# Kernel tuning notes

Measured on AMD Instinct MI355X. Metric: run time of the kernel, lower is better.

Reference implementation:

```python
import jax, jax.numpy as jnp
import numpy as np

D_MODEL = 1024
D_HIDDEN = 4096
NUM_EXPERT = 8
TOP_K = 2
B, N = 1, 8192


def setup_inputs() -> dict:
    key = jax.random.key(0)
    ks = jax.random.split(key, 8)
    s1 = 1.0 / np.sqrt(D_MODEL)
    s2 = 1.0 / np.sqrt(D_HIDDEN)
    return {
        "x": jax.random.normal(ks[0], (B, N, D_MODEL), jnp.float32),
        "expert_tokens": jax.random.normal(ks[1], (NUM_EXPERT, D_MODEL), jnp.float32),
        "W1": jax.random.normal(ks[2], (NUM_EXPERT, D_MODEL, D_HIDDEN), jnp.float32) * s1,
        "b1": jnp.zeros((NUM_EXPERT, D_HIDDEN), jnp.float32),
        "W2": jax.random.normal(ks[3], (NUM_EXPERT, D_HIDDEN, D_HIDDEN), jnp.float32) * s2,
        "b2": jnp.zeros((NUM_EXPERT, D_HIDDEN), jnp.float32),
        "W3": jax.random.normal(ks[4], (NUM_EXPERT, D_HIDDEN, D_MODEL), jnp.float32) * s2,
        "b3": jnp.zeros((NUM_EXPERT, D_MODEL), jnp.float32),
    }


def _expert_mlp(x, W1, b1, W2, b2, W3, b3):
    # Linear -> GELU (exact, matching torch nn.GELU) -> Linear -> GELU -> Linear
    h = jax.nn.gelu(jnp.einsum("bnd,dh->bnh", x, W1) + b1, approximate=False)
    h = jax.nn.gelu(jnp.einsum("bnh,hk->bnk", h, W2) + b2, approximate=False)
    return jnp.einsum("bnh,hd->bnd", h, W3) + b3


def reference(x, expert_tokens, W1, b1, W2, b2, W3, b3):
    # router scores: [B, N, E]
    scores = jnp.einsum("bnd,ed->bne", x, expert_tokens)
    _, topk_idx = jax.lax.top_k(scores, TOP_K)  # [B, N, TOP_K]
    outputs = jnp.zeros_like(x)
    num_expert = W1.shape[0]
    for i in range(num_expert):
        # gate weight = (# of top-k slots assigned to expert i) / top_k
        w = jnp.mean((topk_idx == i).astype(x.dtype), axis=-1, keepdims=True)
        y = _expert_mlp(x, W1[i], b1[i], W2[i], b2[i], W3[i], b3[i])
        outputs = outputs + y * w
    return outputs
```

## Files before the change

### kernel.cpp

```cpp
#include <hip/hip_runtime.h>
#include <stdint.h>

#define D_MODEL 1024
#define D_HID   4096
#define NEXP    8
#define NTOK    8192
#define TOTROW  (NTOK*2)

typedef unsigned short ushort_t;
typedef __attribute__((ext_vector_type(8))) short short8;
typedef __attribute__((ext_vector_type(4))) float f32x4;

static __device__ __forceinline__ ushort_t f2bf(float f) {
    union { float f; uint32_t u; } v; v.f = f;
    uint32_t u = v.u;
    uint32_t r = (u + 0x7FFFu + ((u >> 16) & 1u)) >> 16;
    return (ushort_t)r;
}
static __device__ __forceinline__ float bf2f(ushort_t h) {
    union { uint32_t u; float f; } v; v.u = ((uint32_t)h) << 16;
    return v.f;
}
static __device__ __forceinline__ float gelu_f(float x) {
    return 0.5f * x * (1.0f + erff(x * 0.70710678118654752f));
}

static __device__ __forceinline__ void gload_lds16(const void* g, void* l) {
    __builtin_amdgcn_global_load_lds(
        (const __attribute__((address_space(1))) void*)g,
        (__attribute__((address_space(3))) void*)l,
        16, 0, 0);
}

__global__ __launch_bounds__(256) void router_kernel(
    const float* __restrict__ x, const float* __restrict__ et,
    int* __restrict__ cnt, int* __restrict__ top2)
{
    __shared__ float lds_et[NEXP * D_MODEL];
    int t = threadIdx.x;
    #pragma unroll
    for (int i = 0; i < (NEXP * D_MODEL) / 256; ++i)
        lds_et[i * 256 + t] = et[i * 256 + t];
    __syncthreads();

    int lane = t & 63, wv = t >> 6;
    int n = blockIdx.x * 4 + wv;
    double s[NEXP];
    #pragma unroll
    for (int e = 0; e < NEXP; ++e) s[e] = 0.0;
    const float* xr = x + (size_t)n * D_MODEL;
    for (int it = 0; it < D_MODEL / 64; ++it) {
        float xv = xr[it * 64 + lane];
        #pragma unroll
        for (int e = 0; e < NEXP; ++e)
            s[e] += (double)(xv * lds_et[e * D_MODEL + it * 64 + lane]);
    }
    #pragma unroll
    for (int e = 0; e < NEXP; ++e)
        for (int off = 32; off; off >>= 1)
            s[e] += __shfl_xor(s[e], off);

    if (lane == 0) {
        int e1 = 0;
        for (int e = 1; e < NEXP; ++e) if (s[e] > s[e1]) e1 = e;
        int e2 = (e1 == 0) ? 1 : 0;
        for (int e = 0; e < NEXP; ++e) if (e != e1 && s[e] > s[e2]) e2 = e;
        top2[n * 2 + 0] = e1;
        top2[n * 2 + 1] = e2;
        atomicAdd(&cnt[e1], 1);
        atomicAdd(&cnt[e2], 1);
    }
}

__global__ void scan_kernel(const int* __restrict__ cnt, int* __restrict__ base,
                            int* __restrict__ cnt2)
{
    if (threadIdx.x == 0 && blockIdx.x == 0) {
        int acc = 0;
        for (int e = 0; e < NEXP; ++e) { base[e] = acc; acc += cnt[e]; cnt2[e] = 0; }
    }
}

__global__ __launch_bounds__(256) void assign_kernel(
    const int* __restrict__ top2, const int* __restrict__ base,
    int* __restrict__ cnt2, int* __restrict__ rowinfo, int* __restrict__ token_rows)
{
    int n = blockIdx.x * 256 + threadIdx.x;
    if (n >= NTOK) return;
    #pragma unroll
    for (int k = 0; k < 2; ++k) {
        int e = top2[n * 2 + k];
        int slot = atomicAdd(&cnt2[e], 1);
        int row = base[e] + slot;
        rowinfo[row] = n;
        token_rows[n * 2 + k] = row;
    }
}

__global__ __launch_bounds__(256) void convert_x(
    const float* __restrict__ x, ushort_t* __restrict__ xb)
{
    size_t i = ((size_t)blockIdx.x * 256 + threadIdx.x) * 4;
    float4 f = *(const float4*)(x + i);
    ushort_t o[4];
    o[0] = f2bf(f.x); o[1] = f2bf(f.y); o[2] = f2bf(f.z); o[3] = f2bf(f.w);
    *(uint2*)(xb + i) = *(const uint2*)o;
}

__global__ __launch_bounds__(256) void transpose_kernel(
    const float* __restrict__ in, ushort_t* __restrict__ out, int K, int N)
{
    __shared__ float tile[64][65];
    int e = blockIdx.z;
    int k0 = blockIdx.y * 64, n0 = blockIdx.x * 64;
    const float* ine = in + (size_t)e * K * N + (size_t)k0 * N + n0;
    ushort_t* oute = out + (size_t)e * N * K + (size_t)n0 * K + k0;
    int t = threadIdx.x;
    int lr = t >> 4;
    int lc = (t & 15) * 4;
    #pragma unroll
    for (int i = 0; i < 4; ++i) {
        float4 v = *(const float4*)(ine + (size_t)(i * 16 + lr) * N + lc);
        tile[i * 16 + lr][lc + 0] = v.x;
        tile[i * 16 + lr][lc + 1] = v.y;
        tile[i * 16 + lr][lc + 2] = v.z;
        tile[i * 16 + lr][lc + 3] = v.w;
    }
    __syncthreads();
    int nr = t >> 3;
    int kg = (t & 7) * 8;
    #pragma unroll
    for (int j = 0; j < 2; ++j) {
        int n = j * 32 + nr;
        ushort_t o[8];
        #pragma unroll
        for (int m = 0; m < 8; ++m) o[m] = f2bf(tile[kg + m][n]);
        *(uint4*)(oute + (size_t)n * K + kg) = *(const uint4*)o;
    }
}


#define RD_A(BUF, MH) do {                                                        \
    _Pragma("unroll") for (int mi = 0; mi < 4; ++mi) {                            \
        areg[mi][0] = *(const short8*)(pA0 + (BUF)*16384 + (MH)*4096 + mi*1024);  \
        areg[mi][1] = *(const short8*)(pA1 + (BUF)*16384 + (MH)*4096 + mi*1024);  \
    }                                                                             \
} while (0)

#define RD_B(DST, BUF, NH) do {                                                   \
    _Pragma("unroll") for (int ni = 0; ni < 2; ++ni) {                            \
        DST[ni][0] = *(const short8*)(pB0 + (BUF)*16384 + (NH)*2048 + ni*1024);   \
        DST[ni][1] = *(const short8*)(pB1 + (BUF)*16384 + (NH)*2048 + ni*1024);   \
    }                                                                             \
} while (0)

#define MM(BR, MH, NH) do {                                                       \
    __builtin_amdgcn_s_setprio(1);                                                \
    _Pragma("unroll") for (int mi = 0; mi < 4; ++mi)                              \
    _Pragma("unroll") for (int ni = 0; ni < 2; ++ni)                              \
    _Pragma("unroll") for (int ks = 0; ks < 2; ++ks)                              \
      acc[(MH)*4 + mi][(NH)*2 + ni] = __builtin_amdgcn_mfma_f32_16x16x32_bf16(    \
          areg[mi][ks], BR[ni][ks], acc[(MH)*4 + mi][(NH)*2 + ni], 0, 0, 0);      \
    __builtin_amdgcn_s_setprio(0);                                                \
} while (0)

#define PH(MH, NH, BR, TAIL) do { MM(BR, MH, NH); TAIL; __builtin_amdgcn_s_barrier(); } while (0)

#define VW6 asm volatile("s_waitcnt vmcnt(6)" ::: "memory")
#define VW0 asm volatile("s_waitcnt vmcnt(0)" ::: "memory")

template<bool GATHER, bool GELU_ACT>
__global__ __launch_bounds__(512, 2) void moe_gemm8(
    const ushort_t* __restrict__ Ah,
    const ushort_t* __restrict__ BT,
    const float* __restrict__ bias,
    ushort_t* __restrict__ C,
    const int* __restrict__ cnt, const int* __restrict__ basep,
    const int* __restrict__ rowinfo,
    int Ncols, int K)
{
    const int e = blockIdx.z;
    const int cnte = cnt[e];
    const int mt = blockIdx.y;
    if (mt * 256 >= cnte) return;
    const int base_e = basep[e];
    const int row0 = base_e + mt * 256;
    const int col0 = blockIdx.x * 256;

    __shared__ __attribute__((aligned(16))) ushort_t SMEM[2][2][256][64];

    const int t = threadIdx.x;
    const int lane = t & 63;
    const int wv = t >> 6;
    const int wm = wv >> 2;
    const int wn = wv & 3;
    const int l15 = lane & 15, lhi = lane >> 4;
    const int key = l15 & 7;
    const int lr8 = lane >> 3;
    const int sl  = (lane & 7) ^ lr8;

    const int slot0 = (lhi ^ key) * 8;
    const int slot1 = ((4 + lhi) ^ key) * 8;
    const ushort_t* pA0 = &SMEM[0][0][wm * 128 + l15][slot0];
    const ushort_t* pA1 = &SMEM[0][0][wm * 128 + l15][slot1];
    const ushort_t* pB0 = &SMEM[1][0][wn * 64 + l15][slot0];
    const ushort_t* pB1 = &SMEM[1][0][wn * 64 + l15][slot1];

    uint32_t aOff[2][2], bOff[2][2];
    #pragma unroll
    for (int mh = 0; mh < 2; ++mh)
        #pragma unroll
        for (int c = 0; c < 2; ++c) {
            int tr = mh * 64 + wv * 8 + lr8 + c * 128;
            int gr = row0 + tr; if (gr > TOTROW - 1) gr = TOTROW - 1;
            uint32_t rowid = GATHER ? (uint32_t)rowinfo[gr] : (uint32_t)gr;
            aOff[mh][c] = rowid * (uint32_t)(K * 2) + sl * 16;
        }
    #pragma unroll
    for (int nh = 0; nh < 2; ++nh)
        #pragma unroll
        for (int c = 0; c < 2; ++c) {
            int tr = (wv >> 2) * 64 + nh * 32 + (wv & 3) * 8 + lr8 + c * 128;
            bOff[nh][c] = ((uint32_t)e * Ncols + col0 + tr) * (uint32_t)(K * 2) + sl * 16;
        }

    const int arb = wv * 8;
    const int brb = (wv >> 2) * 64 + (wv & 3) * 8;

    auto stageA = [&](int buf, int mh) {
        gload_lds16((const char*)Ah + aOff[mh][0], (void*)&SMEM[0][buf][mh * 64 + arb][0]);
        gload_lds16((const char*)Ah + aOff[mh][1], (void*)&SMEM[0][buf][128 + mh * 64 + arb][0]);
        aOff[mh][0] += 128; aOff[mh][1] += 128;
    };
    auto stageB = [&](int buf, int nh) {
        gload_lds16((const char*)BT + bOff[nh][0], (void*)&SMEM[1][buf][nh * 32 + brb][0]);
        gload_lds16((const char*)BT + bOff[nh][1], (void*)&SMEM[1][buf][128 + nh * 32 + brb][0]);
        bOff[nh][0] += 128; bOff[nh][1] += 128;
    };

    f32x4 acc[8][4];
    #pragma unroll
    for (int i = 0; i < 8; ++i)
        #pragma unroll
        for (int j = 0; j < 4; ++j)
            acc[i][j] = (f32x4){0.f, 0.f, 0.f, 0.f};

    short8 areg[4][2], breg0[2][2], breg1[2][2];

    const int KT = K / 64;
    const int NIT = KT / 2;

    stageA(0, 0); stageB(0, 0); stageB(0, 1); stageA(0, 1);
    stageA(1, 0); stageB(1, 0); stageB(1, 1); stageA(1, 1);
    VW0;
    __builtin_amdgcn_s_barrier();
    RD_A(0, 0); RD_B(breg0, 0, 0);

    for (int i2 = 0; i2 < NIT - 1; ++i2) {
         PH(0, 0, breg0, { stageA(0, 0); RD_B(breg1, 0, 1); });
         PH(0, 1, breg1, { stageB(0, 0); RD_A(0, 1); });
         PH(1, 1, breg1, { stageB(0, 1); VW6; });
         PH(1, 0, breg0, { stageA(0, 1); RD_A(1, 0); RD_B(breg0, 1, 0); });
         PH(0, 0, breg0, { stageA(1, 0); RD_B(breg1, 1, 1); });
         PH(0, 1, breg1, { stageB(1, 0); RD_A(1, 1); });
         PH(1, 1, breg1, { stageB(1, 1); VW6; });
         PH(1, 0, breg0, { stageA(1, 1); RD_A(0, 0); RD_B(breg0, 0, 0); });
    }
    {
         PH(0, 0, breg0, { RD_B(breg1, 0, 1); });
         PH(0, 1, breg1, { RD_A(0, 1); });
         PH(1, 1, breg1, { VW0; });
         PH(1, 0, breg0, { RD_A(1, 0); RD_B(breg0, 1, 0); });
         PH(0, 0, breg0, { RD_B(breg1, 1, 1); });
         PH(0, 1, breg1, { RD_A(1, 1); });
         PH(1, 1, breg1, { });
         MM(breg0, 1, 0);
    }

    ushort_t* ctile = &SMEM[0][0][0][0];
    #pragma unroll
    for (int n = 0; n < 4; ++n) {
        int c = wn * 64 + n * 16 + l15;
        float bv = bias[e * Ncols + col0 + c];
        #pragma unroll
        for (int m = 0; m < 8; ++m) {
            #pragma unroll
            for (int q = 0; q < 4; ++q) {
                int r = wm * 128 + m * 16 + lhi * 4 + q;
                float v = acc[m][n][q] + bv;
                if (GELU_ACT) v = gelu_f(v);
                ctile[r * 256 + ((c >> 3) ^ ((r & 7) << 2)) * 8 + (c & 7)] = f2bf(v);
            }
        }
    }
    __syncthreads();
    {
        int rr = t >> 2;
        int ch0 = t & 3;
        #pragma unroll
        for (int pass = 0; pass < 2; ++pass) {
            int r = pass * 128 + rr;
            int rl = mt * 256 + r;
            if (rl < cnte) {
                size_t gbase = (size_t)(base_e + rl) * Ncols + col0;
                #pragma unroll
                for (int i = 0; i < 8; ++i) {
                    int ch = ch0 + i * 4;
                    uint4 v = *(const uint4*)&ctile[r * 256 + ((ch ^ ((r & 7) << 2)) * 8)];
                    *(uint4*)&C[gbase + ch * 8] = v;
                }
            }
        }
    }
}

__global__ __launch_bounds__(256) void combine_kernel(
    const ushort_t* __restrict__ Y, const int* __restrict__ token_rows,
    float* __restrict__ out)
{
    int n = blockIdx.x;
    int t = threadIdx.x;
    int r1 = token_rows[n * 2 + 0], r2 = token_rows[n * 2 + 1];
    const ushort_t* y1 = Y + (size_t)r1 * D_MODEL + t * 4;
    const ushort_t* y2 = Y + (size_t)r2 * D_MODEL + t * 4;
    ushort_t a[4], b[4];
    *(uint2*)a = *(const uint2*)y1;
    *(uint2*)b = *(const uint2*)y2;
    float4 o;
    o.x = 0.5f * (bf2f(a[0]) + bf2f(b[0]));
    o.y = 0.5f * (bf2f(a[1]) + bf2f(b[1]));
    o.z = 0.5f * (bf2f(a[2]) + bf2f(b[2]));
    o.w = 0.5f * (bf2f(a[3]) + bf2f(b[3]));
    *(float4*)(out + (size_t)n * D_MODEL + t * 4) = o;
}

extern "C" void kernel_launch(void* const* d_in, const int* in_sizes, int n_in,
                              void* d_out, int out_size, void* d_ws, size_t ws_size,
                              hipStream_t stream)
{
    const float* x  = (const float*)d_in[0];
    const float* et = (const float*)d_in[1];
    const float* W1 = (const float*)d_in[2];
    const float* b1 = (const float*)d_in[3];
    const float* W2 = (const float*)d_in[4];
    const float* b2 = (const float*)d_in[5];
    const float* W3 = (const float*)d_in[6];
    const float* b3 = (const float*)d_in[7];
    float* out = (float*)d_out;

    char* ws = (char*)d_ws;
    size_t off = 0;
    auto alloc = [&](size_t bytes) -> char* {
        char* p = ws + off;
        off += (bytes + 255) & ~(size_t)255;
        return p;
    };
    int* cnt        = (int*)alloc(NEXP * 4);
    int* basep      = (int*)alloc(NEXP * 4);
    int* cnt2       = (int*)alloc(NEXP * 4);
    int* top2       = (int*)alloc((size_t)NTOK * 2 * 4);
    int* token_rows = (int*)alloc((size_t)NTOK * 2 * 4);
    int* rowinfo    = (int*)alloc((size_t)TOTROW * 4);
    ushort_t* W1T = (ushort_t*)alloc((size_t)NEXP * D_HID * D_MODEL * 2);
    ushort_t* W2T = (ushort_t*)alloc((size_t)NEXP * D_HID * D_HID * 2);
    ushort_t* W3T = (ushort_t*)alloc((size_t)NEXP * D_MODEL * D_HID * 2);
    ushort_t* H1  = (ushort_t*)alloc((size_t)TOTROW * D_HID * 2);
    ushort_t* H2  = (ushort_t*)alloc((size_t)TOTROW * D_HID * 2);
    ushort_t* Yr  = (ushort_t*)alloc((size_t)TOTROW * D_MODEL * 2);
    if (off > ws_size) return;

    ushort_t* xb = H2;

    hipMemsetAsync(cnt, 0, NEXP * 4, stream);
    router_kernel<<<NTOK / 4, 256, 0, stream>>>(x, et, cnt, top2);
    scan_kernel<<<1, 64, 0, stream>>>(cnt, basep, cnt2);
    assign_kernel<<<NTOK / 256, 256, 0, stream>>>(top2, basep, cnt2, rowinfo, token_rows);

    convert_x<<<(NTOK * D_MODEL) / 1024, 256, 0, stream>>>(x, xb);

    transpose_kernel<<<dim3(D_HID / 64, D_MODEL / 64, NEXP), 256, 0, stream>>>(W1, W1T, D_MODEL, D_HID);
    transpose_kernel<<<dim3(D_HID / 64, D_HID / 64, NEXP), 256, 0, stream>>>(W2, W2T, D_HID, D_HID);
    transpose_kernel<<<dim3(D_MODEL / 64, D_HID / 64, NEXP), 256, 0, stream>>>(W3, W3T, D_HID, D_MODEL);

    moe_gemm8<true, true><<<dim3(D_HID / 256, 16, NEXP), 512, 0, stream>>>(
        xb, W1T, b1, H1, cnt, basep, rowinfo, D_HID, D_MODEL);
    moe_gemm8<false, true><<<dim3(D_HID / 256, 16, NEXP), 512, 0, stream>>>(
        H1, W2T, b2, H2, cnt, basep, rowinfo, D_HID, D_HID);
    moe_gemm8<false, false><<<dim3(D_MODEL / 256, 16, NEXP), 512, 0, stream>>>(
        H2, W3T, b3, Yr, cnt, basep, rowinfo, D_MODEL, D_HID);

    combine_kernel<<<NTOK, 256, 0, stream>>>(Yr, token_rows, out);
}
```

Before: 1.502 ms.

## Fuse bf16 cast into router, flatten GEMM grid, grid-stride combine

The fp32-to-bf16 conversion of x moves into the router kernel, which already reads x, so one full pass over x and one launch are gone. The MoE GEMM grids become 1D with the expert index in the low bits, so consecutive blocks cover different experts. This spreads work across experts and skips empty tiles early. The combine kernel uses a grid-stride loop with 2048 blocks instead of one block per token. The router's bf16 stores are 2-byte per-lane writes, narrower than the old vectorized conversion.

Result: slower. 1.624 ms (+8.1%).

```diff
diff --git a/kernel.cpp b/kernel.cpp
--- a/kernel.cpp
+++ b/kernel.cpp
@@ -34,7 +34,7 @@
 
 __global__ __launch_bounds__(256) void router_kernel(
     const float* __restrict__ x, const float* __restrict__ et,
-    int* __restrict__ cnt, int* __restrict__ top2)
+    int* __restrict__ cnt, int* __restrict__ top2, ushort_t* __restrict__ xb)
 {
     __shared__ float lds_et[NEXP * D_MODEL];
     int t = threadIdx.x;
@@ -49,8 +49,10 @@
     #pragma unroll
     for (int e = 0; e < NEXP; ++e) s[e] = 0.0;
     const float* xr = x + (size_t)n * D_MODEL;
+    ushort_t* xbr = xb + (size_t)n * D_MODEL;
     for (int it = 0; it < D_MODEL / 64; ++it) {
         float xv = xr[it * 64 + lane];
+        xbr[it * 64 + lane] = f2bf(xv);
         #pragma unroll
         for (int e = 0; e < NEXP; ++e)
             s[e] += (double)(xv * lds_et[e * D_MODEL + it * 64 + lane]);
@@ -97,16 +99,6 @@
     }
 }
 
-__global__ __launch_bounds__(256) void convert_x(
-    const float* __restrict__ x, ushort_t* __restrict__ xb)
-{
-    size_t i = ((size_t)blockIdx.x * 256 + threadIdx.x) * 4;
-    float4 f = *(const float4*)(x + i);
-    ushort_t o[4];
-    o[0] = f2bf(f.x); o[1] = f2bf(f.y); o[2] = f2bf(f.z); o[3] = f2bf(f.w);
-    *(uint2*)(xb + i) = *(const uint2*)o;
-}
-
 __global__ __launch_bounds__(256) void transpose_kernel(
     const float* __restrict__ in, ushort_t* __restrict__ out, int K, int N)
 {
@@ -179,13 +171,16 @@
     const int* __restrict__ rowinfo,
     int Ncols, int K)
 {
-    const int e = blockIdx.z;
+    const int bid = blockIdx.x;
+    const int e  = bid & 7;
+    const int w  = bid >> 3;
+    const int mt = w & 15;
+    const int xt = w >> 4;
     const int cnte = cnt[e];
-    const int mt = blockIdx.y;
     if (mt * 256 >= cnte) return;
     const int base_e = basep[e];
     const int row0 = base_e + mt * 256;
-    const int col0 = blockIdx.x * 256;
+    const int col0 = xt * 256;
 
     __shared__ __attribute__((aligned(16))) ushort_t SMEM[2][2][256][64];
 
@@ -318,20 +313,21 @@
     const ushort_t* __restrict__ Y, const int* __restrict__ token_rows,
     float* __restrict__ out)
 {
-    int n = blockIdx.x;
     int t = threadIdx.x;
-    int r1 = token_rows[n * 2 + 0], r2 = token_rows[n * 2 + 1];
-    const ushort_t* y1 = Y + (size_t)r1 * D_MODEL + t * 4;
-    const ushort_t* y2 = Y + (size_t)r2 * D_MODEL + t * 4;
-    ushort_t a[4], b[4];
-    *(uint2*)a = *(const uint2*)y1;
-    *(uint2*)b = *(const uint2*)y2;
-    float4 o;
-    o.x = 0.5f * (bf2f(a[0]) + bf2f(b[0]));
-    o.y = 0.5f * (bf2f(a[1]) + bf2f(b[1]));
-    o.z = 0.5f * (bf2f(a[2]) + bf2f(b[2]));
-    o.w = 0.5f * (bf2f(a[3]) + bf2f(b[3]));
-    *(float4*)(out + (size_t)n * D_MODEL + t * 4) = o;
+    for (int n = blockIdx.x; n < NTOK; n += gridDim.x) {
+        int r1 = token_rows[n * 2 + 0], r2 = token_rows[n * 2 + 1];
+        const ushort_t* y1 = Y + (size_t)r1 * D_MODEL + t * 4;
+        const ushort_t* y2 = Y + (size_t)r2 * D_MODEL + t * 4;
+        ushort_t a[4], b[4];
+        *(uint2*)a = *(const uint2*)y1;
+        *(uint2*)b = *(const uint2*)y2;
+        float4 o;
+        o.x = 0.5f * (bf2f(a[0]) + bf2f(b[0]));
+        o.y = 0.5f * (bf2f(a[1]) + bf2f(b[1]));
+        o.z = 0.5f * (bf2f(a[2]) + bf2f(b[2]));
+        o.w = 0.5f * (bf2f(a[3]) + bf2f(b[3]));
+        *(float4*)(out + (size_t)n * D_MODEL + t * 4) = o;
+    }
 }
 
 extern "C" void kernel_launch(void* const* d_in, const int* in_sizes, int n_in,
@@ -372,22 +368,20 @@
     ushort_t* xb = H2;
 
     hipMemsetAsync(cnt, 0, NEXP * 4, stream);
-    router_kernel<<<NTOK / 4, 256, 0, stream>>>(x, et, cnt, top2);
+    router_kernel<<<NTOK / 4, 256, 0, stream>>>(x, et, cnt, top2, xb);
     scan_kernel<<<1, 64, 0, stream>>>(cnt, basep, cnt2);
     assign_kernel<<<NTOK / 256, 256, 0, stream>>>(top2, basep, cnt2, rowinfo, token_rows);
-
-    convert_x<<<(NTOK * D_MODEL) / 1024, 256, 0, stream>>>(x, xb);
 
     transpose_kernel<<<dim3(D_HID / 64, D_MODEL / 64, NEXP), 256, 0, stream>>>(W1, W1T, D_MODEL, D_HID);
     transpose_kernel<<<dim3(D_HID / 64, D_HID / 64, NEXP), 256, 0, stream>>>(W2, W2T, D_HID, D_HID);
     transpose_kernel<<<dim3(D_MODEL / 64, D_HID / 64, NEXP), 256, 0, stream>>>(W3, W3T, D_HID, D_MODEL);
 
-    moe_gemm8<true, true><<<dim3(D_HID / 256, 16, NEXP), 512, 0, stream>>>(
+    moe_gemm8<true, true><<<(D_HID / 256) * 16 * NEXP, 512, 0, stream>>>(
         xb, W1T, b1, H1, cnt, basep, rowinfo, D_HID, D_MODEL);
-    moe_gemm8<false, true><<<dim3(D_HID / 256, 16, NEXP), 512, 0, stream>>>(
+    moe_gemm8<false, true><<<(D_HID / 256) * 16 * NEXP, 512, 0, stream>>>(
         H1, W2T, b2, H2, cnt, basep, rowinfo, D_HID, D_HID);
-    moe_gemm8<false, false><<<dim3(D_MODEL / 256, 16, NEXP), 512, 0, stream>>>(
+    moe_gemm8<false, false><<<(D_MODEL / 256) * 16 * NEXP, 512, 0, stream>>>(
         H2, W3T, b3, Yr, cnt, basep, rowinfo, D_MODEL, D_HID);
 
-    combine_kernel<<<NTOK, 256, 0, stream>>>(Yr, token_rows, out);
-}
+    combine_kernel<<<2048, 256, 0, stream>>>(Yr, token_rows, out);
+}
```
